# Kernel optimization log

Hardware: AMD Instinct MI355X
Metric: run time of the kernel (lower is better)

Reference implementation:

```python
import jax, jax.numpy as jnp
import numpy as np

B, L, H, N, NB = 16, 4096, 256, 64, 4
EXPAND = 2


def setup_inputs() -> dict:
    key = jax.random.key(0)
    ks = jax.random.split(key, 12)
    def nrm(k, shape, scale):
        return jax.random.normal(k, shape, dtype=jnp.float32) * scale
    inp = {}
    inp["x"] = jax.random.normal(ks[0], (B, L, 1), dtype=jnp.float32)
    # conv stem: Conv1d(1 -> H, kernel 5, pad 2)
    inp["conv_w"] = nrm(ks[1], (H, 1, 5), 1.0 / np.sqrt(5.0))
    inp["conv_b"] = jnp.zeros((H,), jnp.float32)
    # per-block S4 (S4D diagonal kernel) params, stacked over NB blocks
    inp["s4_norm_w"] = jnp.ones((NB, H), jnp.float32)
    inp["s4_norm_b"] = jnp.zeros((NB, H), jnp.float32)
    inp["log_dt"] = (np.log(0.001) + jax.random.uniform(ks[2], (NB, H), dtype=jnp.float32) * (np.log(0.1) - np.log(0.001))).astype(jnp.float32)
    inp["log_A_real"] = jnp.full((NB, H, N), np.log(0.5), jnp.float32)
    inp["A_imag"] = jnp.tile(np.pi * jnp.arange(N, dtype=jnp.float32), (NB, H, 1))
    inp["C_re"] = nrm(ks[3], (NB, H, N), 0.5 ** 0.5)
    inp["C_im"] = nrm(ks[4], (NB, H, N), 0.5 ** 0.5)
    inp["D"] = nrm(ks[5], (NB, H), 1.0)
    # S4 output GLU linear: H -> 2H, then glu -> H
    inp["s4_out_w"] = nrm(ks[6], (NB, 2 * H, H), 1.0 / np.sqrt(H))
    inp["s4_out_b"] = jnp.zeros((NB, 2 * H), jnp.float32)
    # FF block (expand=2)
    inp["ff_norm_w"] = jnp.ones((NB, H), jnp.float32)
    inp["ff_norm_b"] = jnp.zeros((NB, H), jnp.float32)
    inp["ff_w1"] = nrm(ks[7], (NB, EXPAND * H, H), 1.0 / np.sqrt(H))
    inp["ff_b1"] = jnp.zeros((NB, EXPAND * H), jnp.float32)
    inp["ff_w2"] = nrm(ks[8], (NB, H, EXPAND * H), 1.0 / np.sqrt(EXPAND * H))
    inp["ff_b2"] = jnp.zeros((NB, H), jnp.float32)
    return inp


def _ln_ch(x, w, b):
    # LayerNorm over channel dim of x: [B, H, L] (prenorm on transposed layout)
    mu = jnp.mean(x, axis=1, keepdims=True)
    var = jnp.mean((x - mu) ** 2, axis=1, keepdims=True)
    return (x - mu) * jax.lax.rsqrt(var + 1e-5) * w[None, :, None] + b[None, :, None]


def _s4d_kernel(log_dt, log_A_real, A_imag, C_re, C_im, Lk):
    # Diagonal SSM (S4D) convolution kernel, returns [H, Lk]
    dt = jnp.exp(log_dt)                       # [H]
    A = -jnp.exp(log_A_real) + 1j * A_imag     # [H, N]
    dtA = A * dt[:, None]                      # [H, N]
    C = (C_re + 1j * C_im) * (jnp.exp(dtA) - 1.0) / A
    V = jnp.exp(dtA[:, :, None] * jnp.arange(Lk, dtype=jnp.float32))  # [H, N, Lk]
    return 2.0 * jnp.einsum('hn,hnl->hl', C, V).real


def reference(x, conv_w, conv_b, s4_norm_w, s4_norm_b, log_dt, log_A_real, A_imag,
              C_re, C_im, D, s4_out_w, s4_out_b, ff_norm_w, ff_norm_b,
              ff_w1, ff_b1, ff_w2, ff_b2):
    u = jnp.transpose(x, (0, 2, 1))  # [B, 1, L]
    h = jax.lax.conv_general_dilated(u, conv_w, (1,), [(2, 2)],
                                     dimension_numbers=('NCH', 'OIH', 'NCH'))
    h = h + conv_b[None, :, None]    # [B, H, L]
    Lx = h.shape[-1]
    for i in range(NB):
        # --- S4 residual block (prenorm, FFT long conv, D-skip, GELU, GLU out) ---
        z = _ln_ch(h, s4_norm_w[i], s4_norm_b[i])
        k = _s4d_kernel(log_dt[i], log_A_real[i], A_imag[i], C_re[i], C_im[i], Lx)
        zf = jnp.fft.rfft(z, n=2 * Lx)
        kf = jnp.fft.rfft(k, n=2 * Lx)
        y = jnp.fft.irfft(zf * kf[None], n=2 * Lx)[..., :Lx]
        y = y + z * D[i][None, :, None]
        y = jax.nn.gelu(y, approximate=False)
        y2 = jnp.einsum('fh,bhl->bfl', s4_out_w[i], y) + s4_out_b[i][None, :, None]
        a, g = jnp.split(y2, 2, axis=1)
        h = h + a * jax.nn.sigmoid(g)
        # --- FF residual block (prenorm, pointwise MLP expand=2, GELU) ---
        z = _ln_ch(h, ff_norm_w[i], ff_norm_b[i])
        z = jax.nn.gelu(jnp.einsum('fh,bhl->bfl', ff_w1[i], z) + ff_b1[i][None, :, None], approximate=False)
        z = jnp.einsum('hf,bfl->bhl', ff_w2[i], z) + ff_b2[i][None, :, None]
        h = h + z
    return h[:, :, -1]  # [B, H]
```

## Files before the change

kernel.cpp:

```cpp
#include <hip/hip_runtime.h>
#include <math.h>

#define Bq 16
#define Lq 4096
#define Hq 256
#define Nq 64
#define NBq 4
#define F2q 512
#define BLq (Bq*Lq)

typedef __attribute__((ext_vector_type(8))) short short8;
typedef __attribute__((ext_vector_type(4))) float f32x4;

__device__ __forceinline__ unsigned short f2bf(float f){
  unsigned u = __float_as_uint(f);
  u = (u + 0x7fffu + ((u >> 16) & 1u)) >> 16;
  return (unsigned short)u;
}
__device__ __forceinline__ float bf2f(unsigned short u){
  return __uint_as_float(((unsigned)u) << 16);
}
__device__ __forceinline__ float gelu(float x){
  float u = 0.79788456f*x*(1.f + 0.044715f*x*x);
  float t = 1.f - __fdividef(2.f, 1.f + __expf(2.f*fabsf(u)));
  return 0.5f*x*(1.f + copysignf(t, u));
}

__device__ __forceinline__ void stage16(const void* g, void* l){
  __builtin_amdgcn_global_load_lds((const __attribute__((address_space(1))) void*)g,
                                   (__attribute__((address_space(3))) void*)l, 16, 0, 0);
}

__global__ __launch_bounds__(256) void k_convln(const float* __restrict__ x,
    const float* __restrict__ cw, const float* __restrict__ cb,
    unsigned short* __restrict__ h, float* __restrict__ mu, float* __restrict__ rstd){
  __shared__ float xs[260];
  __shared__ float cwS[Hq*5];
  __shared__ float cbS[Hq];
  const int b = blockIdx.x >> 4;
  const int l0 = (blockIdx.x & 15) * 256;
  const int tid = threadIdx.x;
  for (int i=tid; i<Hq*5; i+=256) cwS[i] = cw[i];
  cbS[tid] = cb[tid];
  {
    int gl = l0 + tid - 2;
    xs[tid] = (gl>=0 && gl<Lq) ? x[(size_t)b*Lq + gl] : 0.f;
    if (tid < 4){
      int gl2 = l0 + 254 + tid;
      xs[256+tid] = (gl2>=0 && gl2<Lq) ? x[(size_t)b*Lq + gl2] : 0.f;
    }
  }
  __syncthreads();
  float s0=0.f, s1=0.f;
  unsigned short* hp = h + (size_t)b*Hq*Lq + l0 + tid;
  for (int c=0;c<Hq;c++){
    float acc = cbS[c];
    #pragma unroll
    for (int k=0;k<5;k++) acc = fmaf(cwS[c*5+k], xs[tid+k], acc);
    hp[(size_t)c*Lq] = f2bf(acc);
    s0 += acc; s1 = fmaf(acc, acc, s1);
  }
  int col = b*Lq + l0 + tid;
  float m = s0 * (1.0f/256.0f);
  float var = s1*(1.0f/256.0f) - m*m;
  mu[col] = m;
  rstd[col] = rsqrtf(fmaxf(var, 0.f) + 1e-5f);
}

__global__ __launch_bounds__(256) void k_s4pre(const float* __restrict__ log_dt,
    const float* __restrict__ lar, const float* __restrict__ aim,
    const float* __restrict__ cre, const float* __restrict__ cim,
    float* __restrict__ wre, float* __restrict__ wim,
    float* __restrict__ c2re, float* __restrict__ c2im){
  int idx = blockIdx.x*256 + threadIdx.x;
  int hh = (idx >> 6) & (Hq-1);
  int i = idx >> 14;
  float dt = expf(log_dt[i*Hq + hh]);
  float are = -expf(lar[idx]);
  float ai  = aim[idx];
  float dre = are*dt, dim = ai*dt;
  float er = expf(dre);
  float wr = er*cosf(dim), wi = er*sinf(dim);
  float nr = wr - 1.f, ni = wi;
  float den = are*are + ai*ai;
  float qre = (nr*are + ni*ai)/den;
  float qim = (ni*are - nr*ai)/den;
  float Cr = cre[idx], Ci = cim[idx];
  float cer = Cr*qre - Ci*qim;
  float cei = Cr*qim + Ci*qre;
  wre[idx] = wr; wim[idx] = wi;
  c2re[idx] = 2.f*cer; c2im[idx] = 2.f*cei;
}

__global__ __launch_bounds__(256) void k_cvtw(const float* __restrict__ s0,
    const float* __restrict__ s1, const float* __restrict__ s2,
    unsigned short* __restrict__ d0, unsigned short* __restrict__ d1,
    unsigned short* __restrict__ d2){
  int idx = blockIdx.x*256 + threadIdx.x;
  d0[idx] = f2bf(s0[idx]);
  d1[idx] = f2bf(s1[idx]);
  d2[idx] = f2bf(s2[idx]);
}

__global__ __launch_bounds__(64) void k_s4mat(const float* __restrict__ wre_,
    const float* __restrict__ wim_, const float* __restrict__ c2re_,
    const float* __restrict__ c2im_, const float* __restrict__ Dp,
    unsigned short* __restrict__ G, unsigned short* __restrict__ Wb,
    float* __restrict__ w64re_, float* __restrict__ w64im_){
  __shared__ float Kv[64];
  const int n = threadIdx.x;
  const int ch = blockIdx.x;
  const int pidx = ch*64 + n;
  const float wr = wre_[pidx], wi = wim_[pidx];
  const float cr = c2re_[pidx], ci = c2im_[pidx];
  unsigned short* Gb = G + (size_t)ch*64*192;
  unsigned short* Wbb = Wb + (size_t)ch*128*64;
  float pre = 1.f, pim = 0.f;
  for (int t=0;t<64;t++){
    float a = cr*pre - ci*pim;
    #pragma unroll
    for (int m=1;m<64;m<<=1) a += __shfl_xor(a, m, 64);
    if (n==0) Kv[t] = a;
    Wbb[n*64 + (63-t)] = f2bf(pre);
    Wbb[(64+n)*64 + (63-t)] = f2bf(pim);
    float qre = pre*wr - pim*wi;
    float qim = pre*wi + pim*wr;
    Gb[t*192 + 64 + n]  = f2bf(cr*qre - ci*qim);
    Gb[t*192 + 128 + n] = f2bf(-(cr*qim + ci*qre));
    pre = qre; pim = qim;
  }
  w64re_[pidx] = pre; w64im_[pidx] = pim;
  __syncthreads();
  float dv = Dp[ch];
  for (int t=0;t<64;t++){
    float kv = (n<=t) ? Kv[t-n] : 0.f;
    if (n==t) kv += dv;
    Gb[t*192 + n] = f2bf(kv);
  }
}

__global__ __launch_bounds__(256) void k_lnfin(const float2* __restrict__ st0,
    const float2* __restrict__ st1, float* __restrict__ mu, float* __restrict__ rstd){
  int col = blockIdx.x*256 + threadIdx.x;
  float2 a = st0[col], b = st1[col];
  float m = (a.x + b.x) * (1.0f/256.0f);
  float var = (a.y + b.y)*(1.0f/256.0f) - m*m;
  mu[col] = m;
  rstd[col] = rsqrtf(fmaxf(var, 0.f) + 1e-5f);
}

__global__ __launch_bounds__(256) void k_prep(const unsigned short* __restrict__ h,
    const float* __restrict__ mu, const float* __restrict__ rstd,
    const float* __restrict__ lnw_, const float* __restrict__ lnb_,
    unsigned short* __restrict__ U, int ib){
  int idx = blockIdx.x*256 + threadIdx.x;
  int l = (idx & 511) * 8;
  int ch = (idx >> 9) & (Hq-1);
  int b = idx >> 17;
  float lw = lnw_[ib*Hq+ch], lb = lnb_[ib*Hq+ch];
  const unsigned short* hp = h + (((size_t)(b*Hq+ch))<<12) + l;
  const float* mp = mu + ((size_t)b<<12) + l;
  const float* rp = rstd + ((size_t)b<<12) + l;
  uint4 hv = *(const uint4*)hp;
  float hf[8];
  hf[0]=bf2f(hv.x&0xffff); hf[1]=bf2f(hv.x>>16);
  hf[2]=bf2f(hv.y&0xffff); hf[3]=bf2f(hv.y>>16);
  hf[4]=bf2f(hv.z&0xffff); hf[5]=bf2f(hv.z>>16);
  hf[6]=bf2f(hv.w&0xffff); hf[7]=bf2f(hv.w>>16);
  unsigned ow[8];
  #pragma unroll
  for (int j=0;j<8;j++){
    float z = (hf[j]-mp[j])*rp[j]*lw + lb;
    ow[j] = f2bf(z);
  }
  uint4 o;
  o.x = ow[0] | (ow[1]<<16); o.y = ow[2] | (ow[3]<<16);
  o.z = ow[4] | (ow[5]<<16); o.w = ow[6] | (ow[7]<<16);
  unsigned short* up = U + ((size_t)ch*1024 + b*64 + (l>>6))*192 + (l&63);
  *(uint4*)up = o;
}

__global__ __launch_bounds__(256,2) void k_bgemm(const unsigned short* __restrict__ Wb,
    const unsigned short* __restrict__ U, unsigned short* __restrict__ Bb){
  __shared__ __align__(16) char smem[34816];
  unsigned short* Alds = (unsigned short*)smem;
  unsigned short* Blds = (unsigned short*)(smem+16384);
  const int tid = threadIdx.x;
  const int lam = tid & 63;
  const int wv = tid >> 6;
  const int wr = wv >> 1, wc = wv & 1;
  const int ch = blockIdx.x;
  const int bc0 = blockIdx.y * 128;
  const unsigned short* Wch = Wb + (size_t)ch*128*64;
  const unsigned short* Uch = U + (size_t)ch*1024*192;
  const int rbase = lam & 15;
  const int kg = lam >> 4;
  const int x7 = lam & 7;
  const int xo0 = ((kg) ^ x7) * 8;
  const int xo1 = ((4+kg) ^ x7) * 8;
  f32x4 acc[4][4] = {};
  #pragma unroll
  for (int c=0;c<4;c++){
    int si = c*256 + tid;
    int row = si >> 3, blk = si & 7;
    int sb = blk ^ (row & 7);
    stage16(Wch + row*64 + sb*8, &Alds[(c*256 + wv*64)*8]);
    stage16(Uch + (size_t)(bc0+row)*192 + sb*8, &Blds[(c*256 + wv*64)*8]);
  }
  __syncthreads();
  #pragma unroll
  for (int kk=0;kk<2;kk++){
    const int xo = kk ? xo1 : xo0;
    short8 af[4], wf[4];
    #pragma unroll
    for (int mf=0;mf<4;mf++)
      af[mf] = *(const short8*)&Alds[(wr*64 + mf*16 + rbase)*64 + xo];
    #pragma unroll
    for (int nf=0;nf<4;nf++)
      wf[nf] = *(const short8*)&Blds[(wc*64 + nf*16 + rbase)*64 + xo];
    #pragma unroll
    for (int mf=0;mf<4;mf++)
      #pragma unroll
      for (int nf=0;nf<4;nf++)
        acc[mf][nf] = __builtin_amdgcn_mfma_f32_16x16x32_bf16(af[mf], wf[nf], acc[mf][nf], 0,0,0);
  }
  __syncthreads();
  unsigned* tru = (unsigned*)smem;
  const int mg = lam >> 4;
  const int ncol = lam & 15;
  #pragma unroll
  for (int nf=0;nf<4;nf++){
    int bcl = wc*64 + nf*16 + ncol;
    #pragma unroll
    for (int mf=0;mf<4;mf++){
      int n2h = wr*32 + mf*8 + mg*2;
      tru[bcl*68 + n2h]     = (unsigned)f2bf(acc[mf][nf][0]) | ((unsigned)f2bf(acc[mf][nf][1])<<16);
      tru[bcl*68 + n2h + 1] = (unsigned)f2bf(acc[mf][nf][2]) | ((unsigned)f2bf(acc[mf][nf][3])<<16);
    }
  }
  __syncthreads();
  {
    int row = tid >> 1, half = tid & 1;
    const unsigned* src = tru + row*68 + half*32;
    unsigned short* dst = Bb + ((size_t)ch*1024 + bc0 + row)*128 + half*64;
    #pragma unroll
    for (int j=0;j<8;j++)
      *(uint4*)(dst + j*8) = *(const uint4*)(src + j*4);
  }
}

__global__ __launch_bounds__(256) void k_cscan(const unsigned short* __restrict__ Bb,
    const float* __restrict__ w64re_, const float* __restrict__ w64im_,
    unsigned short* __restrict__ U){
  const int wid = blockIdx.x*4 + (threadIdx.x >> 6);
  const int n = threadIdx.x & 63;
  const int ch = wid & (Hq-1);
  const int b = wid >> 8;
  const float wr = w64re_[ch*64 + n];
  const float wi = w64im_[ch*64 + n];
  const unsigned short* bp = Bb + ((size_t)ch*1024 + b*64)*128 + n;
  unsigned short* up = U + ((size_t)ch*1024 + b*64)*192;
  float sre = 0.f, sim = 0.f;
  for (int c=0;c<64;c++){
    up[c*192 + 64 + n]  = f2bf(sre);
    up[c*192 + 128 + n] = f2bf(sim);
    float br = bf2f(bp[c*128]), bi = bf2f(bp[c*128 + 64]);
    float t = fmaf(wr, sre, fmaf(-wi, sim, br));
    sim = fmaf(wr, sim, fmaf(wi, sre, bi));
    sre = t;
  }
}

__global__ __launch_bounds__(256,2) void k_ygemm(const unsigned short* __restrict__ G,
    const unsigned short* __restrict__ U, unsigned short* __restrict__ ybuf){
  __shared__ __align__(16) char smem[40960];
  unsigned short* Alds = (unsigned short*)smem;
  unsigned short* Blds = (unsigned short*)(smem + 8192);
  const int tid = threadIdx.x;
  const int lam = tid & 63;
  const int wv = tid >> 6;
  const int ch = blockIdx.x;
  const int col0 = blockIdx.y * 256;
  const unsigned short* Gch = G + (size_t)ch*64*192;
  const unsigned short* Uch = U + (size_t)ch*1024*192;
  const int rbase = lam & 15;
  const int kg = lam >> 4;
  const int x7 = lam & 7;
  const int xo0 = ((kg) ^ x7) * 8;
  const int xo1 = ((4+kg) ^ x7) * 8;
  f32x4 acc[4][4] = {};
  for (int ks=0;ks<3;ks++){
    const int k0 = ks*64;
    #pragma unroll
    for (int c=0;c<2;c++){
      int si = c*256 + tid;
      int row = si >> 3, blk = si & 7;
      int sb = blk ^ (row & 7);
      stage16(Gch + row*192 + k0 + sb*8, &Alds[(c*256 + wv*64)*8]);
    }
    #pragma unroll
    for (int c=0;c<8;c++){
      int si = c*256 + tid;
      int row = si >> 3, blk = si & 7;
      int sb = blk ^ (row & 7);
      stage16(Uch + (size_t)(col0+row)*192 + k0 + sb*8, &Blds[(c*256 + wv*64)*8]);
    }
    __syncthreads();
    #pragma unroll
    for (int kk=0;kk<2;kk++){
      const int xo = kk ? xo1 : xo0;
      short8 af[4], wf[4];
      #pragma unroll
      for (int mf=0;mf<4;mf++)
        af[mf] = *(const short8*)&Alds[(mf*16 + rbase)*64 + xo];
      #pragma unroll
      for (int nf=0;nf<4;nf++)
        wf[nf] = *(const short8*)&Blds[(wv*64 + nf*16 + rbase)*64 + xo];
      #pragma unroll
      for (int mf=0;mf<4;mf++)
        #pragma unroll
        for (int nf=0;nf<4;nf++)
          acc[mf][nf] = __builtin_amdgcn_mfma_f32_16x16x32_bf16(af[mf], wf[nf], acc[mf][nf], 0,0,0);
    }
    __syncthreads();
  }
  unsigned short* trans = (unsigned short*)smem + wv*64*66;
  const int mg = lam >> 4;
  const int ncol = lam & 15;
  #pragma unroll
  for (int mf=0;mf<4;mf++){
    #pragma unroll
    for (int nf=0;nf<4;nf++){
      #pragma unroll
      for (int r=0;r<4;r++){
        int l = mf*16 + mg*4 + r;
        int bcl = nf*16 + ncol;
        trans[bcl*66 + l] = f2bf(gelu(acc[mf][nf][r]));
      }
    }
  }
  __syncthreads();
  const int bc = col0 + wv*64 + lam;
  const int b = bc >> 6, c = bc & 63;
  unsigned short* yp = ybuf + (((size_t)(b*Hq + ch))<<12) + c*64;
  #pragma unroll
  for (int j=0;j<8;j++){
    uint4 v = *(const uint4*)&trans[lam*66 + j*8];
    *(uint4*)(yp + j*8) = v;
  }
}

__global__ __launch_bounds__(256) void k_transp(const unsigned short* __restrict__ src,
    unsigned short* __restrict__ dst){
  __shared__ unsigned lds[64][65];
  const int t = threadIdx.x;
  const int tile = blockIdx.x;
  const int l0 = (tile & 63)*64;
  const int c0 = ((tile>>6)&3)*64;
  const int b = tile >> 8;
  const int rr = t >> 3, c8 = t & 7;
  #pragma unroll
  for (int q=0;q<2;q++){
    int ch = rr + q*32;
    const unsigned short* sp = src + ((size_t)b*Hq + c0+ch)*Lq + l0 + c8*8;
    uint4 v = *(const uint4*)sp;
    lds[ch][c8*8+0] = v.x & 0xffff; lds[ch][c8*8+1] = v.x >> 16;
    lds[ch][c8*8+2] = v.y & 0xffff; lds[ch][c8*8+3] = v.y >> 16;
    lds[ch][c8*8+4] = v.z & 0xffff; lds[ch][c8*8+5] = v.z >> 16;
    lds[ch][c8*8+6] = v.w & 0xffff; lds[ch][c8*8+7] = v.w >> 16;
  }
  __syncthreads();
  #pragma unroll
  for (int q=0;q<2;q++){
    int l = rr + q*32;
    unsigned a[8];
    #pragma unroll
    for (int j=0;j<8;j++) a[j] = lds[c8*8+j][l];
    uint4 o;
    o.x = (a[0]&0xffff) | (a[1]<<16);
    o.y = (a[2]&0xffff) | (a[3]<<16);
    o.z = (a[4]&0xffff) | (a[5]<<16);
    o.w = (a[6]&0xffff) | (a[7]<<16);
    *(uint4*)(dst + ((size_t)b*Lq + l0+l)*Hq + c0 + c8*8) = o;
  }
}

__global__ __launch_bounds__(256) void k_lntransp(const unsigned short* __restrict__ h,
    const float* __restrict__ mu, const float* __restrict__ rstd,
    const float* __restrict__ lnw_, const float* __restrict__ lnb_,
    unsigned short* __restrict__ dst, int ib){
  __shared__ unsigned lds[64][65];
  const int t = threadIdx.x;
  const int tile = blockIdx.x;
  const int l0 = (tile & 63)*64;
  const int c0 = ((tile>>6)&3)*64;
  const int b = tile >> 8;
  const int rr = t >> 3, c8 = t & 7;
  #pragma unroll
  for (int q=0;q<2;q++){
    int ch = c0 + rr + q*32;
    float lw = lnw_[ib*Hq + ch], lb = lnb_[ib*Hq + ch];
    const unsigned short* sp = h + ((size_t)b*Hq + ch)*Lq + l0 + c8*8;
    const float* mp = mu + (size_t)b*Lq + l0 + c8*8;
    const float* rp = rstd + (size_t)b*Lq + l0 + c8*8;
    uint4 hv = *(const uint4*)sp;
    float hf[8];
    hf[0]=bf2f(hv.x&0xffff); hf[1]=bf2f(hv.x>>16);
    hf[2]=bf2f(hv.y&0xffff); hf[3]=bf2f(hv.y>>16);
    hf[4]=bf2f(hv.z&0xffff); hf[5]=bf2f(hv.z>>16);
    hf[6]=bf2f(hv.w&0xffff); hf[7]=bf2f(hv.w>>16);
    #pragma unroll
    for (int j=0;j<8;j++){
      float z = (hf[j] - mp[j]) * rp[j] * lw + lb;
      lds[rr + q*32][c8*8+j] = f2bf(z);
    }
  }
  __syncthreads();
  #pragma unroll
  for (int q=0;q<2;q++){
    int l = rr + q*32;
    unsigned a[8];
    #pragma unroll
    for (int j=0;j<8;j++) a[j] = lds[c8*8+j][l];
    uint4 o;
    o.x = (a[0]&0xffff) | (a[1]<<16);
    o.y = (a[2]&0xffff) | (a[3]<<16);
    o.z = (a[4]&0xffff) | (a[5]<<16);
    o.w = (a[6]&0xffff) | (a[7]<<16);
    *(uint4*)(dst + ((size_t)b*Lq + l0+l)*Hq + c0 + c8*8) = o;
  }
}

template<int MODE, int KDIM>
__global__ __launch_bounds__(256,2) void k_gemm(
    const unsigned short* __restrict__ A, const unsigned short* __restrict__ W,
    const float* __restrict__ bias, unsigned short* __restrict__ h,
    unsigned short* __restrict__ out, float2* __restrict__ stats){
  constexpr int WSH = (MODE==0?2:1)*128*64;
  constexpr int STG_B = (128*64 + WSH)*2;
  constexpr int EPI_B = (MODE==1) ? 128*136*2 : 64*144*4;
  constexpr int SMEM = STG_B > EPI_B ? STG_B : EPI_B;
  __shared__ __align__(16) char smem[SMEM];
  unsigned short* Alds = (unsigned short*)smem;
  unsigned short* Wlds = Alds + 128*64;
  const int tid = threadIdx.x;
  const int lam = tid & 63;
  const int wv = tid >> 6;
  const int wr = wv >> 1, wc = wv & 1;
  const int col0 = blockIdx.x * 128;
  const int n0 = blockIdx.y * 128;
  const int rbase = lam & 15;
  const int kg = lam >> 4;
  const int x7 = lam & 7;
  const int xo0 = ((kg) ^ x7) * 8;
  const int xo1 = ((4+kg) ^ x7) * 8;
  const unsigned short *aP[4], *wP[4], *wP2[4];
  unsigned sDst[4];
  #pragma unroll
  for (int c=0;c<4;c++){
    int si = c*256 + tid;
    int row = si >> 3, blk = si & 7;
    int sb = blk ^ (row & 7);
    aP[c] = A + (size_t)(col0+row)*KDIM + sb*8;
    wP[c] = W + (size_t)(n0+row)*KDIM + sb*8;
    wP2[c] = (MODE==0) ? (W + (size_t)(n0+256+row)*KDIM + sb*8) : nullptr;
    sDst[c] = (unsigned)(c*256 + wv*64)*8;
  }
  f32x4 acc[4][4] = {};
  f32x4 acc2[4][(MODE==0)?4:1] = {};
  for (int k0 = 0; k0 < KDIM; k0 += 64){
    #pragma unroll
    for (int c=0;c<4;c++){
      stage16(aP[c] + k0, &Alds[sDst[c]]);
      stage16(wP[c] + k0, &Wlds[sDst[c]]);
      if constexpr (MODE==0) stage16(wP2[c] + k0, &Wlds[8192 + sDst[c]]);
    }
    __syncthreads();
    #pragma unroll
    for (int kk=0;kk<2;kk++){
      const int xo = kk ? xo1 : xo0;
      short8 af[4], wf[4];
      #pragma unroll
      for (int mf=0;mf<4;mf++)
        af[mf] = *(const short8*)&Alds[(wr*64 + mf*16 + rbase)*64 + xo];
      #pragma unroll
      for (int nf=0;nf<4;nf++)
        wf[nf] = *(const short8*)&Wlds[(wc*64 + nf*16 + rbase)*64 + xo];
      if constexpr (MODE==0){
        short8 wg[4];
        #pragma unroll
        for (int nf=0;nf<4;nf++)
          wg[nf] = *(const short8*)&Wlds[8192 + (wc*64 + nf*16 + rbase)*64 + xo];
        #pragma unroll
        for (int mf=0;mf<4;mf++){
          #pragma unroll
          for (int nf=0;nf<4;nf++){
            acc[mf][nf]  = __builtin_amdgcn_mfma_f32_16x16x32_bf16(af[mf], wf[nf], acc[mf][nf], 0,0,0);
            acc2[mf][nf] = __builtin_amdgcn_mfma_f32_16x16x32_bf16(af[mf], wg[nf], acc2[mf][nf], 0,0,0);
          }
        }
      } else {
        #pragma unroll
        for (int mf=0;mf<4;mf++){
          #pragma unroll
          for (int nf=0;nf<4;nf++)
            acc[mf][nf] = __builtin_amdgcn_mfma_f32_16x16x32_bf16(af[mf], wf[nf], acc[mf][nf], 0,0,0);
        }
      }
    }
    __syncthreads();
  }
  const int mg = lam >> 4;
  const int ncol = lam & 15;
  if constexpr (MODE==1){
    unsigned short* trans = (unsigned short*)smem;
    #pragma unroll
    for (int nf=0;nf<4;nf++){
      int gnl = wc*64 + nf*16 + ncol;
      float bb1 = bias[n0 + gnl];
      #pragma unroll
      for (int mf=0;mf<4;mf++){
        int cl = wr*64 + mf*16 + mg*4;
        #pragma unroll
        for (int r=0;r<4;r++)
          trans[(cl+r)*136 + gnl] = f2bf(gelu(acc[mf][nf][r] + bb1));
      }
    }
    __syncthreads();
    {
      int cl = tid >> 1, gs = (tid & 1)*64;
      const unsigned short* src = trans + cl*136 + gs;
      unsigned short* dst = out + (size_t)(col0+cl)*F2q + n0 + gs;
      #pragma unroll
      for (int j=0;j<8;j++)
        *(uint4*)(dst + j*8) = *(const uint4*)(src + j*8);
    }
  } else {
    float* dlds = (float*)smem;
    const int bb = col0 >> 12;
    const int l0 = col0 & (Lq-1);
    float s0t = 0.f, s1t = 0.f;
    #pragma unroll
    for (int p=0;p<2;p++){
      __syncthreads();
      if (wc == p){
        #pragma unroll
        for (int nf=0;nf<4;nf++){
          int chl = nf*16 + ncol;
          int gn = n0 + p*64 + chl;
          float ba = bias[gn];
          float bg = (MODE==0) ? bias[gn + Hq] : 0.f;
          #pragma unroll
          for (int mf=0;mf<4;mf++){
            int coll = wr*64 + mf*16 + mg*4;
            f32x4 dv;
            #pragma unroll
            for (int r=0;r<4;r++){
              if constexpr (MODE==0){
                float av = acc[mf][nf][r] + ba;
                float gv = acc2[mf][nf][r] + bg;
                dv[r] = __fdividef(av, 1.f + __expf(-gv));
              } else {
                dv[r] = acc[mf][nf][r] + ba;
              }
            }
            *(f32x4*)&dlds[chl*144 + (coll>>5)*36 + (coll&31)] = dv;
          }
        }
      }
      __syncthreads();
      {
        int chl = tid >> 2, seg = tid & 3;
        unsigned short* hp = h + ((size_t)bb*Hq + n0 + p*64 + chl)*Lq + l0 + seg*32;
        float* dp = dlds + chl*144 + seg*36;
        #pragma unroll
        for (int j=0;j<4;j++){
          uint4 hv = *(uint4*)(hp + j*8);
          f32x4 d0 = *(const f32x4*)(dp + j*8);
          f32x4 d1 = *(const f32x4*)(dp + j*8 + 4);
          d0[0] += bf2f(hv.x&0xffff); d0[1] += bf2f(hv.x>>16);
          d0[2] += bf2f(hv.y&0xffff); d0[3] += bf2f(hv.y>>16);
          d1[0] += bf2f(hv.z&0xffff); d1[1] += bf2f(hv.z>>16);
          d1[2] += bf2f(hv.w&0xffff); d1[3] += bf2f(hv.w>>16);
          hv.x = (unsigned)f2bf(d0[0]) | ((unsigned)f2bf(d0[1])<<16);
          hv.y = (unsigned)f2bf(d0[2]) | ((unsigned)f2bf(d0[3])<<16);
          hv.z = (unsigned)f2bf(d1[0]) | ((unsigned)f2bf(d1[1])<<16);
          hv.w = (unsigned)f2bf(d1[2]) | ((unsigned)f2bf(d1[3])<<16);
          *(uint4*)(hp + j*8) = hv;
          *(f32x4*)(dp + j*8) = d0;
          *(f32x4*)(dp + j*8 + 4) = d1;
        }
      }
      __syncthreads();
      {
        int j = tid >> 1, hc = (tid & 1)*32;
        int js = (j>>5)*36 + (j&31);
        float s0 = 0.f, s1 = 0.f;
        #pragma unroll
        for (int c=0;c<32;c++){
          float v = dlds[(hc+c)*144 + js];
          s0 += v; s1 = fmaf(v, v, s1);
        }
        s0 += __shfl_xor(s0, 1, 64);
        s1 += __shfl_xor(s1, 1, 64);
        s0t += s0; s1t += s1;
      }
    }
    if (!(tid & 1)){
      float2* stP = stats + (size_t)blockIdx.y*BLq;
      stP[col0 + (tid >> 1)] = make_float2(s0t, s1t);
    }
  }
}

__global__ __launch_bounds__(256) void k_gather(const unsigned short* __restrict__ h,
    float* __restrict__ o){
  int idx = blockIdx.x*256 + threadIdx.x;
  int b = idx >> 8, c = idx & (Hq-1);
  o[idx] = bf2f(h[((size_t)b*Hq + c)*Lq + (Lq-1)]);
}

extern "C" void kernel_launch(void* const* d_in, const int* in_sizes, int n_in,
                              void* d_out, int out_size, void* d_ws, size_t ws_size,
                              hipStream_t stream) {
  (void)in_sizes; (void)n_in; (void)out_size; (void)ws_size;
  const float* x         = (const float*)d_in[0];
  const float* conv_w    = (const float*)d_in[1];
  const float* conv_b    = (const float*)d_in[2];
  const float* s4_norm_w = (const float*)d_in[3];
  const float* s4_norm_b = (const float*)d_in[4];
  const float* log_dt    = (const float*)d_in[5];
  const float* log_A_real= (const float*)d_in[6];
  const float* A_imag    = (const float*)d_in[7];
  const float* C_re      = (const float*)d_in[8];
  const float* C_im      = (const float*)d_in[9];
  const float* Dp        = (const float*)d_in[10];
  const float* s4_out_w  = (const float*)d_in[11];
  const float* s4_out_b  = (const float*)d_in[12];
  const float* ff_norm_w = (const float*)d_in[13];
  const float* ff_norm_b = (const float*)d_in[14];
  const float* ff_w1     = (const float*)d_in[15];
  const float* ff_b1     = (const float*)d_in[16];
  const float* ff_w2     = (const float*)d_in[17];
  const float* ff_b2     = (const float*)d_in[18];

  char* ws = (char*)d_ws;
  size_t off = 0;
  auto nxt = [&](size_t bytes){ size_t o = off; off = (off + bytes + 255) & ~(size_t)255; return o; };
  unsigned short* h = (unsigned short*)(ws + nxt((size_t)Bq*Hq*Lq*2));
  float* mu     = (float*)(ws + nxt((size_t)BLq*4));
  float* rstd   = (float*)(ws + nxt((size_t)BLq*4));
  float* wre    = (float*)(ws + nxt((size_t)NBq*Hq*Nq*4));
  float* wim    = (float*)(ws + nxt((size_t)NBq*Hq*Nq*4));
  float* c2re   = (float*)(ws + nxt((size_t)NBq*Hq*Nq*4));
  float* c2im   = (float*)(ws + nxt((size_t)NBq*Hq*Nq*4));
  float* w64re  = (float*)(ws + nxt((size_t)NBq*Hq*Nq*4));
  float* w64im  = (float*)(ws + nxt((size_t)NBq*Hq*Nq*4));
  unsigned short* s4wb = (unsigned short*)(ws + nxt((size_t)NBq*F2q*Hq*2));
  unsigned short* f1b  = (unsigned short*)(ws + nxt((size_t)NBq*F2q*Hq*2));
  unsigned short* f2b  = (unsigned short*)(ws + nxt((size_t)NBq*Hq*F2q*2));
  unsigned short* Gm   = (unsigned short*)(ws + nxt((size_t)Hq*64*192*2));
  unsigned short* Wbar = (unsigned short*)(ws + nxt((size_t)Hq*128*64*2));
  unsigned short* U    = (unsigned short*)(ws + nxt((size_t)Hq*1024*192*2));
  unsigned short* Bb   = (unsigned short*)(ws + nxt((size_t)Hq*128*1024*2));
  unsigned short* ybuf = Bb;
  unsigned short* yT   = Bb + (size_t)16*1024*1024;
  unsigned short* zT   = yT;
  unsigned short* z2T  = U;
  float2* st0 = (float2*)Bb;
  float2* st1 = st0 + BLq;

  k_convln<<<Bq*16, 256, 0, stream>>>(x, conv_w, conv_b, h, mu, rstd);
  k_s4pre<<<(NBq*Hq*Nq)/256, 256, 0, stream>>>(log_dt, log_A_real, A_imag, C_re, C_im,
                                               wre, wim, c2re, c2im);
  k_cvtw<<<(NBq*F2q*Hq)/256, 256, 0, stream>>>(s4_out_w, ff_w1, ff_w2, s4wb, f1b, f2b);

  for (int i=0;i<NBq;i++){
    const size_t po = (size_t)i*Hq*Nq;
    k_s4mat<<<Hq, 64, 0, stream>>>(wre+po, wim+po, c2re+po, c2im+po, Dp + i*Hq,
                                   Gm, Wbar, w64re+po, w64im+po);
    k_prep<<<(Bq*Hq*Lq/8)/256, 256, 0, stream>>>(h, mu, rstd, s4_norm_w, s4_norm_b, U, i);
    k_bgemm<<<dim3(Hq, 8), 256, 0, stream>>>(Wbar, U, Bb);
    k_cscan<<<(Bq*Hq)/4, 256, 0, stream>>>(Bb, w64re+po, w64im+po, U);
    k_ygemm<<<dim3(Hq, 4), 256, 0, stream>>>(Gm, U, ybuf);
    k_transp<<<Bq*4*64, 256, 0, stream>>>(ybuf, yT);
    k_gemm<0,256><<<dim3(BLq/128, 2), 256, 0, stream>>>(
        yT, s4wb + (size_t)i*F2q*Hq, s4_out_b + (size_t)i*F2q, h, nullptr, st0);
    k_lnfin<<<BLq/256, 256, 0, stream>>>(st0, st1, mu, rstd);
    k_lntransp<<<Bq*4*64, 256, 0, stream>>>(h, mu, rstd, ff_norm_w, ff_norm_b, zT, i);
    k_gemm<1,256><<<dim3(BLq/128, 4), 256, 0, stream>>>(
        zT, f1b + (size_t)i*F2q*Hq, ff_b1 + (size_t)i*F2q, nullptr, z2T, nullptr);
    k_gemm<2,512><<<dim3(BLq/128, 2), 256, 0, stream>>>(
        z2T, f2b + (size_t)i*Hq*F2q, ff_b2 + (size_t)i*Hq, h, nullptr, st0);
    k_lnfin<<<BLq/256, 256, 0, stream>>>(st0, st1, mu, rstd);
  }
  k_gather<<<(Bq*Hq)/256, 256, 0, stream>>>(h, (float*)d_out);
}
```

Before: 1.180 ms.

## Fuse chunk-state scan into y-GEMM and shrink U buffer to input-only

```diff
diff --git a/kernel.cpp b/kernel.cpp
--- a/kernel.cpp
+++ b/kernel.cpp
@@ -125,8 +125,9 @@
     Wbb[(64+n)*64 + (63-t)] = f2bf(pim);
     float qre = pre*wr - pim*wi;
     float qim = pre*wi + pim*wr;
-    Gb[t*192 + 64 + n]  = f2bf(cr*qre - ci*qim);
-    Gb[t*192 + 128 + n] = f2bf(-(cr*qim + ci*qre));
+    unsigned pk = (unsigned)f2bf(cr*qre - ci*qim)
+                | ((unsigned)f2bf(-(cr*qim + ci*qre)) << 16);
+    *(unsigned*)&Gb[t*192 + 64 + 2*n] = pk;
     pre = qre; pim = qim;
   }
   w64re_[pidx] = pre; w64im_[pidx] = pim;
@@ -176,7 +177,7 @@
   uint4 o;
   o.x = ow[0] | (ow[1]<<16); o.y = ow[2] | (ow[3]<<16);
   o.z = ow[4] | (ow[5]<<16); o.w = ow[6] | (ow[7]<<16);
-  unsigned short* up = U + ((size_t)ch*1024 + b*64 + (l>>6))*192 + (l&63);
+  unsigned short* up = U + ((size_t)ch*1024 + b*64 + (l>>6))*64 + (l&63);
   *(uint4*)up = o;
 }
 
@@ -192,7 +193,7 @@
   const int ch = blockIdx.x;
   const int bc0 = blockIdx.y * 128;
   const unsigned short* Wch = Wb + (size_t)ch*128*64;
-  const unsigned short* Uch = U + (size_t)ch*1024*192;
+  const unsigned short* Uch = U + (size_t)ch*1024*64;
   const int rbase = lam & 15;
   const int kg = lam >> 4;
   const int x7 = lam & 7;
@@ -205,7 +206,7 @@
     int row = si >> 3, blk = si & 7;
     int sb = blk ^ (row & 7);
     stage16(Wch + row*64 + sb*8, &Alds[(c*256 + wv*64)*8]);
-    stage16(Uch + (size_t)(bc0+row)*192 + sb*8, &Blds[(c*256 + wv*64)*8]);
+    stage16(Uch + (size_t)(bc0+row)*64 + sb*8, &Blds[(c*256 + wv*64)*8]);
   }
   __syncthreads();
   #pragma unroll
@@ -249,104 +250,100 @@
   }
 }
 
-__global__ __launch_bounds__(256) void k_cscan(const unsigned short* __restrict__ Bb,
+__global__ __launch_bounds__(256,2) void k_ygemm(const unsigned short* __restrict__ G,
+    const unsigned short* __restrict__ Uz, const unsigned short* __restrict__ Bb,
     const float* __restrict__ w64re_, const float* __restrict__ w64im_,
-    unsigned short* __restrict__ U){
-  const int wid = blockIdx.x*4 + (threadIdx.x >> 6);
-  const int n = threadIdx.x & 63;
-  const int ch = wid & (Hq-1);
-  const int b = wid >> 8;
-  const float wr = w64re_[ch*64 + n];
-  const float wi = w64im_[ch*64 + n];
-  const unsigned short* bp = Bb + ((size_t)ch*1024 + b*64)*128 + n;
-  unsigned short* up = U + ((size_t)ch*1024 + b*64)*192;
-  float sre = 0.f, sim = 0.f;
-  for (int c=0;c<64;c++){
-    up[c*192 + 64 + n]  = f2bf(sre);
-    up[c*192 + 128 + n] = f2bf(sim);
-    float br = bf2f(bp[c*128]), bi = bf2f(bp[c*128 + 64]);
-    float t = fmaf(wr, sre, fmaf(-wi, sim, br));
-    sim = fmaf(wr, sim, fmaf(wi, sre, bi));
-    sre = t;
-  }
-}
-
-__global__ __launch_bounds__(256,2) void k_ygemm(const unsigned short* __restrict__ G,
-    const unsigned short* __restrict__ U, unsigned short* __restrict__ ybuf){
-  __shared__ __align__(16) char smem[40960];
-  unsigned short* Alds = (unsigned short*)smem;
-  unsigned short* Blds = (unsigned short*)(smem + 8192);
+    unsigned short* __restrict__ ybuf){
+  __shared__ __align__(16) char smem[65536];
+  unsigned short* Glds  = (unsigned short*)smem;
+  unsigned short* Blds  = (unsigned short*)(smem + 24576);
+  unsigned short* BbPre = (unsigned short*)(smem + 49152);
+  unsigned short* trans = BbPre;
   const int tid = threadIdx.x;
   const int lam = tid & 63;
   const int wv = tid >> 6;
   const int ch = blockIdx.x;
-  const int col0 = blockIdx.y * 256;
+  const int b = blockIdx.y;
   const unsigned short* Gch = G + (size_t)ch*64*192;
-  const unsigned short* Uch = U + (size_t)ch*1024*192;
-  const int rbase = lam & 15;
-  const int kg = lam >> 4;
-  const int x7 = lam & 7;
-  const int xo0 = ((kg) ^ x7) * 8;
-  const int xo1 = ((4+kg) ^ x7) * 8;
-  f32x4 acc[4][4] = {};
+  const unsigned short* Uch = Uz + ((size_t)ch*1024 + b*64)*64;
+  const unsigned short* Bch = Bb + ((size_t)ch*1024 + b*64)*128;
+  #pragma unroll
   for (int ks=0;ks<3;ks++){
-    const int k0 = ks*64;
     #pragma unroll
     for (int c=0;c<2;c++){
       int si = c*256 + tid;
       int row = si >> 3, blk = si & 7;
       int sb = blk ^ (row & 7);
-      stage16(Gch + row*192 + k0 + sb*8, &Alds[(c*256 + wv*64)*8]);
-    }
-    #pragma unroll
-    for (int c=0;c<8;c++){
-      int si = c*256 + tid;
-      int row = si >> 3, blk = si & 7;
-      int sb = blk ^ (row & 7);
-      stage16(Uch + (size_t)(col0+row)*192 + k0 + sb*8, &Blds[(c*256 + wv*64)*8]);
-    }
-    __syncthreads();
+      stage16(Gch + row*192 + ks*64 + sb*8, &Glds[ks*4096 + (c*256 + wv*64)*8]);
+    }
+  }
+  #pragma unroll
+  for (int c=0;c<2;c++){
+    int si = c*256 + tid;
+    int row = si >> 3, blk = si & 7;
+    int sb = blk ^ (row & 7);
+    stage16(Uch + row*64 + sb*8, &Blds[(c*256 + wv*64)*8]);
+  }
+  #pragma unroll
+  for (int c=0;c<4;c++){
+    int si = c*256 + tid;
+    stage16(Bch + (si>>4)*128 + (si&15)*8, &BbPre[(c*256 + wv*64)*8]);
+  }
+  __syncthreads();
+  if (wv == 0){
+    const float wr64 = w64re_[ch*64 + lam];
+    const float wi64 = w64im_[ch*64 + lam];
+    const int pos = 2*lam;
+    const int base = 4096 + (pos>>6)*4096;
+    const int pp = pos & 63;
+    float sre = 0.f, sim = 0.f;
+    for (int c=0;c<64;c++){
+      unsigned pk = (unsigned)f2bf(sre) | ((unsigned)f2bf(sim)<<16);
+      int swz = (((pp>>3) ^ (c&7))<<3) + (pp&7);
+      *(unsigned*)&Blds[base + c*64 + swz] = pk;
+      float br = bf2f(BbPre[c*128 + lam]);
+      float bi = bf2f(BbPre[c*128 + 64 + lam]);
+      float t = fmaf(wr64, sre, fmaf(-wi64, sim, br));
+      sim = fmaf(wr64, sim, fmaf(wi64, sre, bi));
+      sre = t;
+    }
+  }
+  __syncthreads();
+  const int rbase = lam & 15;
+  const int kg = lam >> 4;
+  const int x7 = lam & 7;
+  f32x4 acc[4] = {};
+  #pragma unroll
+  for (int ks=0;ks<3;ks++){
     #pragma unroll
     for (int kk=0;kk<2;kk++){
-      const int xo = kk ? xo1 : xo0;
-      short8 af[4], wf[4];
+      const int xo = ((kk*4 + kg) ^ x7) * 8;
+      short8 wfr = *(const short8*)&Blds[ks*4096 + (wv*16 + rbase)*64 + xo];
       #pragma unroll
-      for (int mf=0;mf<4;mf++)
-        af[mf] = *(const short8*)&Alds[(mf*16 + rbase)*64 + xo];
-      #pragma unroll
-      for (int nf=0;nf<4;nf++)
-        wf[nf] = *(const short8*)&Blds[(wv*64 + nf*16 + rbase)*64 + xo];
-      #pragma unroll
-      for (int mf=0;mf<4;mf++)
-        #pragma unroll
-        for (int nf=0;nf<4;nf++)
-          acc[mf][nf] = __builtin_amdgcn_mfma_f32_16x16x32_bf16(af[mf], wf[nf], acc[mf][nf], 0,0,0);
-    }
-    __syncthreads();
-  }
-  unsigned short* trans = (unsigned short*)smem + wv*64*66;
+      for (int mf=0;mf<4;mf++){
+        short8 afr = *(const short8*)&Glds[ks*4096 + (mf*16 + rbase)*64 + xo];
+        acc[mf] = __builtin_amdgcn_mfma_f32_16x16x32_bf16(afr, wfr, acc[mf], 0,0,0);
+      }
+    }
+  }
   const int mg = lam >> 4;
   const int ncol = lam & 15;
+  const int cn = wv*16 + ncol;
   #pragma unroll
   for (int mf=0;mf<4;mf++){
     #pragma unroll
-    for (int nf=0;nf<4;nf++){
-      #pragma unroll
-      for (int r=0;r<4;r++){
-        int l = mf*16 + mg*4 + r;
-        int bcl = nf*16 + ncol;
-        trans[bcl*66 + l] = f2bf(gelu(acc[mf][nf][r]));
-      }
-    }
-  }
-  __syncthreads();
-  const int bc = col0 + wv*64 + lam;
-  const int b = bc >> 6, c = bc & 63;
-  unsigned short* yp = ybuf + (((size_t)(b*Hq + ch))<<12) + c*64;
-  #pragma unroll
-  for (int j=0;j<8;j++){
-    uint4 v = *(const uint4*)&trans[lam*66 + j*8];
-    *(uint4*)(yp + j*8) = v;
+    for (int r=0;r<4;r++){
+      int l = mf*16 + mg*4 + r;
+      trans[cn*72 + l] = f2bf(gelu(acc[mf][r]));
+    }
+  }
+  __syncthreads();
+  {
+    int cc = tid >> 2, seg = tid & 3;
+    unsigned short* yp = ybuf + (((size_t)(b*Hq + ch))<<12) + cc*64 + seg*16;
+    const unsigned short* src = trans + cc*72 + seg*16;
+    *(uint4*)yp = *(const uint4*)src;
+    *(uint4*)(yp+8) = *(const uint4*)(src+8);
   }
 }
 
@@ -661,12 +658,13 @@
   unsigned short* f2b  = (unsigned short*)(ws + nxt((size_t)NBq*Hq*F2q*2));
   unsigned short* Gm   = (unsigned short*)(ws + nxt((size_t)Hq*64*192*2));
   unsigned short* Wbar = (unsigned short*)(ws + nxt((size_t)Hq*128*64*2));
-  unsigned short* U    = (unsigned short*)(ws + nxt((size_t)Hq*1024*192*2));
+  unsigned short* U    = (unsigned short*)(ws + nxt((size_t)Hq*1024*64*2));
   unsigned short* Bb   = (unsigned short*)(ws + nxt((size_t)Hq*128*1024*2));
-  unsigned short* ybuf = Bb;
-  unsigned short* yT   = Bb + (size_t)16*1024*1024;
-  unsigned short* zT   = yT;
-  unsigned short* z2T  = U;
+  unsigned short* ZBUF = (unsigned short*)(ws + nxt((size_t)BLq*F2q*2));
+  unsigned short* yT   = ZBUF;
+  unsigned short* ybuf = ZBUF + (size_t)16*1024*1024;
+  unsigned short* z2T  = ZBUF;
+  unsigned short* zT   = Bb + (size_t)16*1024*1024;
   float2* st0 = (float2*)Bb;
   float2* st1 = st0 + BLq;
 
@@ -681,8 +679,7 @@
                                    Gm, Wbar, w64re+po, w64im+po);
     k_prep<<<(Bq*Hq*Lq/8)/256, 256, 0, stream>>>(h, mu, rstd, s4_norm_w, s4_norm_b, U, i);
     k_bgemm<<<dim3(Hq, 8), 256, 0, stream>>>(Wbar, U, Bb);
-    k_cscan<<<(Bq*Hq)/4, 256, 0, stream>>>(Bb, w64re+po, w64im+po, U);
-    k_ygemm<<<dim3(Hq, 4), 256, 0, stream>>>(Gm, U, ybuf);
+    k_ygemm<<<dim3(Hq, Bq), 256, 0, stream>>>(Gm, U, Bb, w64re+po, w64im+po, ybuf);
     k_transp<<<Bq*4*64, 256, 0, stream>>>(ybuf, yT);
     k_gemm<0,256><<<dim3(BLq/128, 2), 256, 0, stream>>>(
         yT, s4wb + (size_t)i*F2q*Hq, s4_out_b + (size_t)i*F2q, h, nullptr, st0);
```

Result: no change. 1.191 ms (+0.9%).
